# Kernel optimization log

Measured on AMD Instinct MI355X. Metric: run time of the kernel, lower is better.

Reference implementation:

```python
import jax, jax.numpy as jnp
import numpy as np

GAMMA = 267.52  # gyromagnetic ratio constant used as default in forward


def make_laplacian_kernel(vox=(1.0, 1.0, 1.0)):
    vx, vy, vz = vox
    mx, my, mz = 1.0 / vx ** 2, 1.0 / vy ** 2, 1.0 / vz ** 2
    mv = -2.0 * (mx + my + mz)
    k = np.zeros((3, 3, 3), dtype=np.float32)
    # layout matches the torch conv_op nested list: k[d, h, w]
    k[0, 1, 1] = mz
    k[2, 1, 1] = mz
    k[1, 0, 1] = mx
    k[1, 2, 1] = mx
    k[1, 1, 0] = my
    k[1, 1, 2] = my
    k[1, 1, 1] = mv
    return jnp.asarray(k)[None, None]  # [O=1, I=1, 3, 3, 3]


def lg(x, kernel):
    # conv3d, stride 1, padding 1 (SAME for 3^3 kernel), NCDHW
    out = jax.lax.conv_general_dilated(
        x, kernel, window_strides=(1, 1, 1), padding=[(1, 1)] * 3,
        dimension_numbers=('NCDHW', 'OIDHW', 'NCDHW'))
    # zero the boundary slices along each spatial dim (matches LG)
    out = out.at[:, :, 0, :, :].set(0.0).at[:, :, -1, :, :].set(0.0)
    out = out.at[:, :, :, 0, :].set(0.0).at[:, :, :, -1, :].set(0.0)
    out = out.at[:, :, :, :, 0].set(0.0).at[:, :, :, :, -1].set(0.0)
    return out


def setup_inputs() -> dict:
    key = jax.random.key(0)
    k1, k2 = jax.random.split(key)
    B, C, H, W, D = 2, 1, 256, 256, 128
    phi = jax.random.normal(k1, (B, C, H, W, D), dtype=jnp.float32)
    lfs = jax.random.normal(k2, (B, C, H, W, D), dtype=jnp.float32) * 0.01
    mask = jnp.ones((B, C, H, W, D), dtype=jnp.float32)
    TE = jax.random.uniform(jax.random.fold_in(key, 1), (B,), dtype=jnp.float32) * 0.02 + 0.005
    B0 = jnp.full((1,), 3.0, dtype=jnp.float32)
    kernel = make_laplacian_kernel((1.0, 1.0, 1.0))
    return {"phi": phi, "lfs": lfs, "mask": mask, "TE": TE, "B0": B0, "kernel": kernel}


def reference(phi, lfs, mask, TE, B0, kernel):
    expPhi_r = jnp.cos(phi)
    expPhi_i = jnp.sin(phi)
    a_r = lg(expPhi_r, kernel)
    a_i = lg(expPhi_i, kernel)
    b_i = (a_i * expPhi_r - a_r * expPhi_i) * mask
    te = TE[:, None, None, None, None]  # broadcast over [B,1,H,W,D]
    b_i = -b_i / (B0 * te * GAMMA)
    d_i = lg(lfs, kernel) * mask
    return (b_i, d_i)
```

## Files before the change

### kernel.cpp

```cpp
#include <hip/hip_runtime.h>

#define GAMMA_F 267.52f
typedef float v4f __attribute__((ext_vector_type(4)));

constexpr int H = 256, W = 256, D = 128;
constexpr int WT = 8;
constexpr int HS = 16;
constexpr int LW = WT + 2;
constexpr int LD = D + 4;
constexpr long long sW = D;
constexpr long long sH = (long long)W * D;
constexpr long long sB = (long long)H * (long long)W * D;

__global__ __launch_bounds__(256) void lot_lds_march(
    const float* __restrict__ phi,
    const float* __restrict__ lfs,
    const float* __restrict__ mask,
    const float* __restrict__ TE,
    const float* __restrict__ B0,
    const float* __restrict__ kern,
    float* __restrict__ out_b,
    float* __restrict__ out_d)
{
    __shared__ float Ssin[3][LW][LD];
    __shared__ float Scos[3][LW][LD];

    const int tid = threadIdx.x;
    const int q   = tid & 31;
    const int wr  = tid >> 5;
    const int w0  = blockIdx.x * WT;
    const int h0  = blockIdx.y * HS;
    const int b   = blockIdx.z;
    const int w   = w0 + wr;
    const int d0  = q * 4;
    const int lwc = wr + 1;

    const long long colBase = (long long)b * sB + (long long)w * sW + d0;

    const float kHc = kern[4];
    const float kWc = kern[10];
    const float kDc = kern[12];
    const float kCc = kern[13];
    const float scale = -1.0f / (B0[0] * TE[b] * GAMMA_F);

    const bool haloLo  = (wr == 0)      && (w0 > 0);
    const bool haloHi  = (wr == WT - 1) && (w0 + WT < W);
    const bool hasHalo = haloLo || haloHi;
    const long long haloOff = haloLo ? -sW : sW;
    const int  haloLw  = haloLo ? 0 : (LW - 1);

    #define PHI_LOAD(hh, PREG, PHREG)                                        \
    do {                                                                     \
        const int _h = (hh);                                                 \
        if (_h >= 0 && _h < H) {                                             \
            const long long _r = colBase + (long long)_h * sH;               \
            PREG = *(const v4f*)(phi + _r);                                  \
            if (hasHalo) PHREG = *(const v4f*)(phi + _r + haloOff);          \
        }                                                                    \
    } while (0)

    #define PHI_STORE(SLOT, PREG, PHREG)                                     \
    do {                                                                     \
        const int _s = (SLOT);                                               \
        Ssin[_s][lwc][d0 + 1] = __sinf(PREG.x);                              \
        Ssin[_s][lwc][d0 + 2] = __sinf(PREG.y);                              \
        Ssin[_s][lwc][d0 + 3] = __sinf(PREG.z);                              \
        Ssin[_s][lwc][d0 + 4] = __sinf(PREG.w);                              \
        Scos[_s][lwc][d0 + 1] = __cosf(PREG.x);                              \
        Scos[_s][lwc][d0 + 2] = __cosf(PREG.y);                              \
        Scos[_s][lwc][d0 + 3] = __cosf(PREG.z);                              \
        Scos[_s][lwc][d0 + 4] = __cosf(PREG.w);                              \
        if (hasHalo) {                                                       \
            Ssin[_s][haloLw][d0 + 1] = __sinf(PHREG.x);                      \
            Ssin[_s][haloLw][d0 + 2] = __sinf(PHREG.y);                      \
            Ssin[_s][haloLw][d0 + 3] = __sinf(PHREG.z);                      \
            Ssin[_s][haloLw][d0 + 4] = __sinf(PHREG.w);                      \
            Scos[_s][haloLw][d0 + 1] = __cosf(PHREG.x);                      \
            Scos[_s][haloLw][d0 + 2] = __cosf(PHREG.y);                      \
            Scos[_s][haloLw][d0 + 3] = __cosf(PHREG.z);                      \
            Scos[_s][haloLw][d0 + 4] = __cosf(PHREG.w);                      \
        }                                                                    \
    } while (0)

    #define LFS_LOAD(hh, F)                                                  \
    do {                                                                     \
        const int _h = (hh);                                                 \
        if (_h >= 0 && _h < H) {                                             \
            const long long _r = colBase + (long long)_h * sH;               \
            const v4f _l = *(const v4f*)(lfs + _r);                          \
            F[1] = _l.x; F[2] = _l.y; F[3] = _l.z; F[4] = _l.w;              \
            F[0] = (d0 > 0)     ? lfs[_r - 1] : 0.f;                         \
            F[5] = (d0 + 4 < D) ? lfs[_r + 4] : 0.f;                         \
        } else {                                                             \
            _Pragma("unroll")                                                \
            for (int _j = 0; _j < 6; ++_j) F[_j] = 0.f;                      \
        }                                                                    \
    } while (0)

    float FlA[6], FlB[6], FlC[6];
    v4f pT = {0.f, 0.f, 0.f, 0.f}, pTH = {0.f, 0.f, 0.f, 0.f};

    PHI_LOAD(h0 - 1, pT, pTH);
    PHI_STORE(0, pT, pTH);
    PHI_LOAD(h0, pT, pTH);
    PHI_STORE(1, pT, pTH);
    LFS_LOAD(h0 - 1, FlA);
    LFS_LOAD(h0,     FlB);
    v4f pN = pT, pNH = pTH;
    PHI_LOAD(h0 + 1, pN, pNH);

    int sm = 0, sc = 1, sp = 2;

    for (int i = 0; i < HS; ++i) {
        const int h = h0 + i;

        PHI_STORE(sp, pN, pNH);
        LFS_LOAD(h + 1, FlC);
        __syncthreads();

        v4f pN2 = pN, pN2H = pNH;
        PHI_LOAD(h + 2, pN2, pN2H);

        const long long r = colBase + (long long)h * sH;
        if (h == 0 || h == H - 1 || w == 0 || w == W - 1) {
            const v4f z = {0.f, 0.f, 0.f, 0.f};
            __builtin_nontemporal_store(z, (v4f*)(out_b + r));
            __builtin_nontemporal_store(z, (v4f*)(out_d + r));
        } else {
            const v4f lw0 = *(const v4f*)(lfs + r - sW);
            const v4f lw1 = *(const v4f*)(lfs + r + sW);
            const v4f mk  = *(const v4f*)(mask + r);
            const float lwv0[4] = {lw0.x, lw0.y, lw0.z, lw0.w};
            const float lwv1[4] = {lw1.x, lw1.y, lw1.z, lw1.w};
            const float mkv[4]  = {mk.x, mk.y, mk.z, mk.w};

            float ob[4], od[4];
            #pragma unroll
            for (int j = 0; j < 4; ++j) {
                const int di = d0 + 1 + j;
                const float se = Ssin[sc][lwc][di];
                const float ce = Scos[sc][lwc][di];
                const float a_r = kCc * ce
                    + kDc * (Scos[sc][lwc][di - 1] + Scos[sc][lwc][di + 1])
                    + kWc * (Scos[sc][lwc - 1][di] + Scos[sc][lwc + 1][di])
                    + kHc * (Scos[sm][lwc][di]     + Scos[sp][lwc][di]);
                const float a_i = kCc * se
                    + kDc * (Ssin[sc][lwc][di - 1] + Ssin[sc][lwc][di + 1])
                    + kWc * (Ssin[sc][lwc - 1][di] + Ssin[sc][lwc + 1][di])
                    + kHc * (Ssin[sm][lwc][di]     + Ssin[sp][lwc][di]);
                float bi = (a_i * ce - a_r * se) * mkv[j] * scale;

                const float lap = kCc * FlB[j + 1]
                    + kDc * (FlB[j] + FlB[j + 2])
                    + kWc * (lwv0[j] + lwv1[j])
                    + kHc * (FlA[j + 1] + FlC[j + 1]);
                float dv = lap * mkv[j];

                const int d = d0 + j;
                if (d == 0 || d == D - 1) { bi = 0.f; dv = 0.f; }
                ob[j] = bi; od[j] = dv;
            }
            const v4f vb = {ob[0], ob[1], ob[2], ob[3]};
            const v4f vd = {od[0], od[1], od[2], od[3]};
            __builtin_nontemporal_store(vb, (v4f*)(out_b + r));
            __builtin_nontemporal_store(vd, (v4f*)(out_d + r));
        }

        pN = pN2; pNH = pN2H;
        #pragma unroll
        for (int j2 = 0; j2 < 6; ++j2) { FlA[j2] = FlB[j2]; FlB[j2] = FlC[j2]; }
        const int t = sm; sm = sc; sc = sp; sp = t;

        __syncthreads();
    }

    #undef PHI_LOAD
    #undef PHI_STORE
    #undef LFS_LOAD
}

extern "C" void kernel_launch(void* const* d_in, const int* in_sizes, int n_in,
                              void* d_out, int out_size, void* d_ws, size_t ws_size,
                              hipStream_t stream) {
    const float* phi  = (const float*)d_in[0];
    const float* lfs  = (const float*)d_in[1];
    const float* mask = (const float*)d_in[2];
    const float* TE   = (const float*)d_in[3];
    const float* B0   = (const float*)d_in[4];
    const float* kern = (const float*)d_in[5];

    float* out_b = (float*)d_out;
    float* out_d = out_b + sB * 2;

    dim3 grid(W / WT, H / HS, 2);
    dim3 block(256);
    hipLaunchKernelGGL(lot_lds_march, grid, block, 0, stream,
                       phi, lfs, mask, TE, B0, kern, out_b, out_d);
}
```

Baseline: 66.94 us.

## Vectorize LDS access and use wave shuffles for depth-neighbor sin/cos

Drops the padded depth halo in shared memory and writes and reads sin/cos planes with 128-bit vector LDS operations instead of many scalar accesses. The centre-row sin/cos values stay in registers across iterations, and the depth neighbours come from lane shuffles within each 32-lane row group. The aim is to cut LDS instruction count and bank traffic in the stencil, which is now the main non-memory cost. A launch-bounds occupancy hint is also added, which may constrain register allocation.

After: 65.90 us. No clear change (-1.6%).

```diff
diff --git a/kernel.cpp b/kernel.cpp
--- a/kernel.cpp
+++ b/kernel.cpp
@@ -7,12 +7,11 @@
 constexpr int WT = 8;
 constexpr int HS = 16;
 constexpr int LW = WT + 2;
-constexpr int LD = D + 4;
 constexpr long long sW = D;
 constexpr long long sH = (long long)W * D;
 constexpr long long sB = (long long)H * (long long)W * D;
 
-__global__ __launch_bounds__(256) void lot_lds_march(
+__global__ __launch_bounds__(256, 4) void lot_lds_v2(
     const float* __restrict__ phi,
     const float* __restrict__ lfs,
     const float* __restrict__ mask,
@@ -22,8 +21,8 @@
     float* __restrict__ out_b,
     float* __restrict__ out_d)
 {
-    __shared__ float Ssin[3][LW][LD];
-    __shared__ float Scos[3][LW][LD];
+    __shared__ float Ssin[3][LW][D];
+    __shared__ float Scos[3][LW][D];
 
     const int tid = threadIdx.x;
     const int q   = tid & 31;
@@ -49,36 +48,32 @@
     const long long haloOff = haloLo ? -sW : sW;
     const int  haloLw  = haloLo ? 0 : (LW - 1);
 
-    #define PHI_LOAD(hh, PREG, PHREG)                                        \
+    #define PHI_LOAD(hh, P, PH)                                              \
     do {                                                                     \
         const int _h = (hh);                                                 \
         if (_h >= 0 && _h < H) {                                             \
             const long long _r = colBase + (long long)_h * sH;               \
-            PREG = *(const v4f*)(phi + _r);                                  \
-            if (hasHalo) PHREG = *(const v4f*)(phi + _r + haloOff);          \
+            P = *(const v4f*)(phi + _r);                                     \
+            if (hasHalo) PH = *(const v4f*)(phi + _r + haloOff);             \
         }                                                                    \
     } while (0)
 
-    #define PHI_STORE(SLOT, PREG, PHREG)                                     \
+    #define SINCOS_STORE(SLOT, P, PH, SN, CS)                                \
     do {                                                                     \
         const int _s = (SLOT);                                               \
-        Ssin[_s][lwc][d0 + 1] = __sinf(PREG.x);                              \
-        Ssin[_s][lwc][d0 + 2] = __sinf(PREG.y);                              \
-        Ssin[_s][lwc][d0 + 3] = __sinf(PREG.z);                              \
-        Ssin[_s][lwc][d0 + 4] = __sinf(PREG.w);                              \
-        Scos[_s][lwc][d0 + 1] = __cosf(PREG.x);                              \
-        Scos[_s][lwc][d0 + 2] = __cosf(PREG.y);                              \
-        Scos[_s][lwc][d0 + 3] = __cosf(PREG.z);                              \
-        Scos[_s][lwc][d0 + 4] = __cosf(PREG.w);                              \
+        SN[0] = __sinf(P.x); SN[1] = __sinf(P.y);                            \
+        SN[2] = __sinf(P.z); SN[3] = __sinf(P.w);                            \
+        CS[0] = __cosf(P.x); CS[1] = __cosf(P.y);                            \
+        CS[2] = __cosf(P.z); CS[3] = __cosf(P.w);                            \
+        v4f _vs = {SN[0], SN[1], SN[2], SN[3]};                              \
+        v4f _vc = {CS[0], CS[1], CS[2], CS[3]};                              \
+        *(v4f*)&Ssin[_s][lwc][d0] = _vs;                                     \
+        *(v4f*)&Scos[_s][lwc][d0] = _vc;                                     \
         if (hasHalo) {                                                       \
-            Ssin[_s][haloLw][d0 + 1] = __sinf(PHREG.x);                      \
-            Ssin[_s][haloLw][d0 + 2] = __sinf(PHREG.y);                      \
-            Ssin[_s][haloLw][d0 + 3] = __sinf(PHREG.z);                      \
-            Ssin[_s][haloLw][d0 + 4] = __sinf(PHREG.w);                      \
-            Scos[_s][haloLw][d0 + 1] = __cosf(PHREG.x);                      \
-            Scos[_s][haloLw][d0 + 2] = __cosf(PHREG.y);                      \
-            Scos[_s][haloLw][d0 + 3] = __cosf(PHREG.z);                      \
-            Scos[_s][haloLw][d0 + 4] = __cosf(PHREG.w);                      \
+            v4f _hs = {__sinf(PH.x), __sinf(PH.y), __sinf(PH.z), __sinf(PH.w)}; \
+            v4f _hc = {__cosf(PH.x), __cosf(PH.y), __cosf(PH.z), __cosf(PH.w)}; \
+            *(v4f*)&Ssin[_s][haloLw][d0] = _hs;                              \
+            *(v4f*)&Scos[_s][haloLw][d0] = _hc;                              \
         }                                                                    \
     } while (0)
 
@@ -97,16 +92,16 @@
         }                                                                    \
     } while (0)
 
-    float FlA[6], FlB[6], FlC[6];
-    v4f pT = {0.f, 0.f, 0.f, 0.f}, pTH = {0.f, 0.f, 0.f, 0.f};
-
-    PHI_LOAD(h0 - 1, pT, pTH);
-    PHI_STORE(0, pT, pTH);
-    PHI_LOAD(h0, pT, pTH);
-    PHI_STORE(1, pT, pTH);
-    LFS_LOAD(h0 - 1, FlA);
-    LFS_LOAD(h0,     FlB);
-    v4f pN = pT, pNH = pTH;
+    v4f pN  = {0.f, 0.f, 0.f, 0.f}, pNH  = {0.f, 0.f, 0.f, 0.f};
+    float snC[4], csC[4], snT[4], csT[4];
+    float FA[6], FB[6], FC[6];
+
+    PHI_LOAD(h0 - 1, pN, pNH);
+    SINCOS_STORE(0, pN, pNH, snT, csT);
+    PHI_LOAD(h0, pN, pNH);
+    SINCOS_STORE(1, pN, pNH, snC, csC);
+    LFS_LOAD(h0 - 1, FA);
+    LFS_LOAD(h0,     FB);
     PHI_LOAD(h0 + 1, pN, pNH);
 
     int sm = 0, sc = 1, sp = 2;
@@ -114,8 +109,8 @@
     for (int i = 0; i < HS; ++i) {
         const int h = h0 + i;
 
-        PHI_STORE(sp, pN, pNH);
-        LFS_LOAD(h + 1, FlC);
+        SINCOS_STORE(sp, pN, pNH, snT, csT);
+        LFS_LOAD(h + 1, FC);
         __syncthreads();
 
         v4f pN2 = pN, pN2H = pNH;
@@ -127,33 +122,55 @@
             __builtin_nontemporal_store(z, (v4f*)(out_b + r));
             __builtin_nontemporal_store(z, (v4f*)(out_d + r));
         } else {
+            const v4f swm = *(const v4f*)&Ssin[sc][lwc - 1][d0];
+            const v4f swp = *(const v4f*)&Ssin[sc][lwc + 1][d0];
+            const v4f shm = *(const v4f*)&Ssin[sm][lwc][d0];
+            const v4f shp = *(const v4f*)&Ssin[sp][lwc][d0];
+            const v4f cwm = *(const v4f*)&Scos[sc][lwc - 1][d0];
+            const v4f cwp = *(const v4f*)&Scos[sc][lwc + 1][d0];
+            const v4f chm = *(const v4f*)&Scos[sm][lwc][d0];
+            const v4f chp = *(const v4f*)&Scos[sp][lwc][d0];
+
+            const float snL = __shfl_up(snC[3], 1, 32);
+            const float snR = __shfl_down(snC[0], 1, 32);
+            const float csL = __shfl_up(csC[3], 1, 32);
+            const float csR = __shfl_down(csC[0], 1, 32);
+            const float snx[6] = {snL, snC[0], snC[1], snC[2], snC[3], snR};
+            const float csx[6] = {csL, csC[0], csC[1], csC[2], csC[3], csR};
+
             const v4f lw0 = *(const v4f*)(lfs + r - sW);
             const v4f lw1 = *(const v4f*)(lfs + r + sW);
             const v4f mk  = *(const v4f*)(mask + r);
             const float lwv0[4] = {lw0.x, lw0.y, lw0.z, lw0.w};
             const float lwv1[4] = {lw1.x, lw1.y, lw1.z, lw1.w};
             const float mkv[4]  = {mk.x, mk.y, mk.z, mk.w};
+            const float swmv[4] = {swm.x, swm.y, swm.z, swm.w};
+            const float swpv[4] = {swp.x, swp.y, swp.z, swp.w};
+            const float shmv[4] = {shm.x, shm.y, shm.z, shm.w};
+            const float shpv[4] = {shp.x, shp.y, shp.z, shp.w};
+            const float cwmv[4] = {cwm.x, cwm.y, cwm.z, cwm.w};
+            const float cwpv[4] = {cwp.x, cwp.y, cwp.z, cwp.w};
+            const float chmv[4] = {chm.x, chm.y, chm.z, chm.w};
+            const float chpv[4] = {chp.x, chp.y, chp.z, chp.w};
 
             float ob[4], od[4];
             #pragma unroll
             for (int j = 0; j < 4; ++j) {
-                const int di = d0 + 1 + j;
-                const float se = Ssin[sc][lwc][di];
-                const float ce = Scos[sc][lwc][di];
+                const float se = snx[j + 1], ce = csx[j + 1];
                 const float a_r = kCc * ce
-                    + kDc * (Scos[sc][lwc][di - 1] + Scos[sc][lwc][di + 1])
-                    + kWc * (Scos[sc][lwc - 1][di] + Scos[sc][lwc + 1][di])
-                    + kHc * (Scos[sm][lwc][di]     + Scos[sp][lwc][di]);
+                    + kDc * (csx[j] + csx[j + 2])
+                    + kWc * (cwmv[j] + cwpv[j])
+                    + kHc * (chmv[j] + chpv[j]);
                 const float a_i = kCc * se
-                    + kDc * (Ssin[sc][lwc][di - 1] + Ssin[sc][lwc][di + 1])
-                    + kWc * (Ssin[sc][lwc - 1][di] + Ssin[sc][lwc + 1][di])
-                    + kHc * (Ssin[sm][lwc][di]     + Ssin[sp][lwc][di]);
+                    + kDc * (snx[j] + snx[j + 2])
+                    + kWc * (swmv[j] + swpv[j])
+                    + kHc * (shmv[j] + shpv[j]);
                 float bi = (a_i * ce - a_r * se) * mkv[j] * scale;
 
-                const float lap = kCc * FlB[j + 1]
-                    + kDc * (FlB[j] + FlB[j + 2])
+                const float lap = kCc * FB[j + 1]
+                    + kDc * (FB[j] + FB[j + 2])
                     + kWc * (lwv0[j] + lwv1[j])
-                    + kHc * (FlA[j + 1] + FlC[j + 1]);
+                    + kHc * (FA[j + 1] + FC[j + 1]);
                 float dv = lap * mkv[j];
 
                 const int d = d0 + j;
@@ -166,16 +183,18 @@
             __builtin_nontemporal_store(vd, (v4f*)(out_d + r));
         }
 
+        #pragma unroll
+        for (int j2 = 0; j2 < 4; ++j2) { snC[j2] = snT[j2]; csC[j2] = csT[j2]; }
+        #pragma unroll
+        for (int j2 = 0; j2 < 6; ++j2) { FA[j2] = FB[j2]; FB[j2] = FC[j2]; }
         pN = pN2; pNH = pN2H;
-        #pragma unroll
-        for (int j2 = 0; j2 < 6; ++j2) { FlA[j2] = FlB[j2]; FlB[j2] = FlC[j2]; }
         const int t = sm; sm = sc; sc = sp; sp = t;
 
         __syncthreads();
     }
 
     #undef PHI_LOAD
-    #undef PHI_STORE
+    #undef SINCOS_STORE
     #undef LFS_LOAD
 }
 
@@ -194,6 +213,6 @@
 
     dim3 grid(W / WT, H / HS, 2);
     dim3 block(256);
-    hipLaunchKernelGGL(lot_lds_march, grid, block, 0, stream,
+    hipLaunchKernelGGL(lot_lds_v2, grid, block, 0, stream,
                        phi, lfs, mask, TE, B0, kern, out_b, out_d);
 }
```
